# Performance work log

Hardware: AMD Instinct MI355X
Metric: run time of the kernel (lower is better)

The kernel has to match this reference:

```python
import jax, jax.numpy as jnp
import numpy as np

D = 128      # internal_dimensions
L = 4        # num_edge_convs
N = 100000   # nodes
E = 800000   # edges
G = 64       # graphs
IN = 4       # in_channels


def _ln(x, g, b):
    m = jnp.mean(x, -1, keepdims=True)
    v = jnp.mean((x - m) ** 2, -1, keepdims=True)
    return (x - m) * jax.lax.rsqrt(v + 1e-5) * g + b


def _gelu(x):
    return jax.nn.gelu(x, approximate=False)  # torch nn.GELU default (erf)


def _seg_mean(x, seg, n):
    s = jax.ops.segment_sum(x, seg, num_segments=n)
    c = jax.ops.segment_sum(jnp.ones((x.shape[0], 1), x.dtype), seg, num_segments=n)
    return s / jnp.maximum(c, 1.0)


def _seg_max(x, seg, n):
    m = jax.ops.segment_max(x, seg, num_segments=n)
    return jnp.where(jnp.isfinite(m), m, 0.0)  # empty segments -> 0 (PyG convention)


def _forward(x, edge_index, batch, num_graphs,
             in_W1, in_b1, in_g1, in_bn1, in_W2, in_b2, in_g2, in_bn2,
             pre_g, pre_b, cW1, cb1, cg1, cbb1, cW2, cb2, cg2, cbb2, pW, pb,
             ag_g, ag_b,
             kW1, kb1, kg1, kbb1, kW2, kb2, kg2, kbb2,
             kW3, kb3, kg3, kbb3, kW4, kb4):
    n = x.shape[0]
    # input_net: Linear -> LN -> GELU -> Linear -> LN   (dropout=0, eval)
    h = _gelu(_ln(x @ in_W1 + in_b1, in_g1, in_bn1))
    h = _ln(h @ in_W2 + in_b2, in_g2, in_bn2)

    x_in_max = _seg_max(h, batch, num_graphs)
    x_in_mean = _seg_mean(h, batch, num_graphs)

    src, dst = edge_index[0], edge_index[1]  # PyG: message from src (x_j) to dst (x_i)
    xcur = h
    for l in range(L):
        identity = xcur
        hn = _ln(xcur, pre_g[l], pre_b[l])
        xi = hn[dst]            # [E, D]
        xj = hn[src]            # [E, D]
        m = jnp.concatenate([xi, xj - xi], axis=-1)       # [E, 2D]
        m = _gelu(_ln(m @ cW1[l] + cb1[l], cg1[l], cbb1[l]))
        m = _gelu(_ln(m @ cW2[l] + cb2[l], cg2[l], cbb2[l]))
        a_max = _seg_max(m, dst, n)
        a_mean = _seg_mean(m, dst, n)
        aggr = jnp.concatenate([a_max, a_mean], axis=-1)  # [N, 2D]
        xcur = identity + aggr @ pW[l] + pb[l]

    xcur = _ln(xcur, ag_g, ag_b)
    x_g_max = _seg_max(xcur, batch, num_graphs)
    x_g_mean = _seg_mean(xcur, batch, num_graphs)

    xp = jnp.concatenate([x_in_max, x_in_mean, x_g_max, x_g_mean], axis=-1)  # [G, 4D]
    z = _gelu(_ln(xp @ kW1 + kb1, kg1, kbb1))
    z = _gelu(_ln(z @ kW2 + kb2, kg2, kbb2))
    z = _gelu(_ln(z @ kW3 + kb3, kg3, kbb3))
    return z @ kW4 + kb4  # [G, 1]


def setup_inputs() -> dict:
    key = jax.random.key(0)
    ks = iter(jax.random.split(key, 64))
    def W(shape, fan):
        return jax.random.normal(next(ks), shape, jnp.float32) * np.float32((2.0 / fan) ** 0.5)
    inp = {}
    inp["x"] = jax.random.normal(next(ks), (N, IN), jnp.float32)
    inp["edge_index"] = jax.random.randint(next(ks), (2, E), 0, N)
    inp["batch"] = jnp.sort(jax.random.randint(next(ks), (N,), 0, G))
    inp["num_graphs"] = G
    inp["in_W1"] = W((IN, D), IN); inp["in_b1"] = jnp.zeros((D,), jnp.float32)
    inp["in_g1"] = jnp.ones((D,), jnp.float32); inp["in_bn1"] = jnp.zeros((D,), jnp.float32)
    inp["in_W2"] = W((D, D), D); inp["in_b2"] = jnp.zeros((D,), jnp.float32)
    inp["in_g2"] = jnp.ones((D,), jnp.float32); inp["in_bn2"] = jnp.zeros((D,), jnp.float32)
    inp["pre_g"] = jnp.ones((L, D), jnp.float32); inp["pre_b"] = jnp.zeros((L, D), jnp.float32)
    inp["cW1"] = W((L, 2 * D, D), 2 * D); inp["cb1"] = jnp.zeros((L, D), jnp.float32)
    inp["cg1"] = jnp.ones((L, D), jnp.float32); inp["cbb1"] = jnp.zeros((L, D), jnp.float32)
    inp["cW2"] = W((L, D, D), D); inp["cb2"] = jnp.zeros((L, D), jnp.float32)
    inp["cg2"] = jnp.ones((L, D), jnp.float32); inp["cbb2"] = jnp.zeros((L, D), jnp.float32)
    inp["pW"] = W((L, 2 * D, D), 2 * D); inp["pb"] = jnp.zeros((L, D), jnp.float32)
    inp["ag_g"] = jnp.ones((D,), jnp.float32); inp["ag_b"] = jnp.zeros((D,), jnp.float32)
    inp["kW1"] = W((4 * D, D), 4 * D); inp["kb1"] = jnp.zeros((D,), jnp.float32)
    inp["kg1"] = jnp.ones((D,), jnp.float32); inp["kbb1"] = jnp.zeros((D,), jnp.float32)
    inp["kW2"] = W((D, D), D); inp["kb2"] = jnp.zeros((D,), jnp.float32)
    inp["kg2"] = jnp.ones((D,), jnp.float32); inp["kbb2"] = jnp.zeros((D,), jnp.float32)
    inp["kW3"] = W((D, D // 4), D); inp["kb3"] = jnp.zeros((D // 4,), jnp.float32)
    inp["kg3"] = jnp.ones((D // 4,), jnp.float32); inp["kbb3"] = jnp.zeros((D // 4,), jnp.float32)
    inp["kW4"] = W((D // 4, 1), D // 4); inp["kb4"] = jnp.zeros((1,), jnp.float32)
    return inp


def reference(x, edge_index, batch, num_graphs,
              in_W1, in_b1, in_g1, in_bn1, in_W2, in_b2, in_g2, in_bn2,
              pre_g, pre_b, cW1, cb1, cg1, cbb1, cW2, cb2, cg2, cbb2, pW, pb,
              ag_g, ag_b,
              kW1, kb1, kg1, kbb1, kW2, kb2, kg2, kbb2,
              kW3, kb3, kg3, kbb3, kW4, kb4):
    return _forward(x, edge_index, batch, num_graphs,
                    in_W1, in_b1, in_g1, in_bn1, in_W2, in_b2, in_g2, in_bn2,
                    pre_g, pre_b, cW1, cb1, cg1, cbb1, cW2, cb2, cg2, cbb2, pW, pb,
                    ag_g, ag_b,
                    kW1, kb1, kg1, kbb1, kW2, kb2, kg2, kbb2,
                    kW3, kb3, kg3, kbb3, kW4, kb4)
```

## Files before the change

kernel.cpp:

```cpp
#include <hip/hip_runtime.h>
#include <hip/hip_bf16.h>
#include <math.h>

__device__ __forceinline__ float geluf(float x) {
    return 0.5f * x * (1.0f + erff(x * 0.70710678118654752f));
}
#define MAPNEGINF 0x007FFFFFu
__device__ __forceinline__ float funmap(unsigned m) {
    return __uint_as_float((m & 0x80000000u) ? (m ^ 0x80000000u) : ~m);
}
__device__ __forceinline__ unsigned fmap(float f) {
    unsigned u = __float_as_uint(f);
    return ((int)u < 0) ? ~u : (u | 0x80000000u);
}
__device__ __forceinline__ float wred64(float v) {
#pragma unroll
    for (int m = 1; m < 64; m <<= 1) v += __shfl_xor(v, m);
    return v;
}
__device__ __forceinline__ unsigned short bf16r(float f) {
    unsigned u = __float_as_uint(f);
    u += 0x7fffu + ((u >> 16) & 1u);
    return (unsigned short)(u >> 16);
}

__device__ __forceinline__ void stage_wq(float* Ws, const float* __restrict__ src, int t) {
#pragma unroll
    for (int it = 0; it < 4; ++it) {
        const int idx = it * 1024 + (t << 2);
        *(float4*)(Ws + idx) = *(const float4*)(src + idx);
    }
}

__device__ __forceinline__ void kloop_q(const float* As, const float* Ws, float (&acc)[4][8],
                                        const int r0, const int ogc, const int kb) {
#pragma unroll
    for (int kk = 0; kk < 32; kk += 4) {
        const float4 a0 = *(const float4*)(As + (r0 + 0) * 132 + kb + kk);
        const float4 a1 = *(const float4*)(As + (r0 + 1) * 132 + kb + kk);
        const float4 a2 = *(const float4*)(As + (r0 + 2) * 132 + kb + kk);
        const float4 a3 = *(const float4*)(As + (r0 + 3) * 132 + kb + kk);
#define MAD8(R, AV)                                                                     \
    {                                                                                   \
        acc[R][0] += (AV)*wA.x; acc[R][1] += (AV)*wA.y; acc[R][2] += (AV)*wA.z;         \
        acc[R][3] += (AV)*wA.w; acc[R][4] += (AV)*wB.x; acc[R][5] += (AV)*wB.y;         \
        acc[R][6] += (AV)*wB.z; acc[R][7] += (AV)*wB.w;                                 \
    }
#define KSTEP(J, C)                                                                     \
    {                                                                                   \
        const float4 wA = *(const float4*)(Ws + (kk + (J)) * 128 + ogc);                \
        const float4 wB = *(const float4*)(Ws + (kk + (J)) * 128 + 64 + ogc);           \
        MAD8(0, a0.C) MAD8(1, a1.C) MAD8(2, a2.C) MAD8(3, a3.C)                         \
    }
        KSTEP(0, x) KSTEP(1, y) KSTEP(2, z) KSTEP(3, w)
#undef KSTEP
#undef MAD8
    }
}

__global__ void k_zero(unsigned* __restrict__ p, int n) {
    const int i = blockIdx.x * 256 + threadIdx.x;
    if (i < n) p[i] = 0u;
}

__global__ void k_copyu(const unsigned* __restrict__ a, const unsigned* __restrict__ b,
                        unsigned* __restrict__ ac, unsigned* __restrict__ bc, int n) {
    const int i = blockIdx.x * 256 + threadIdx.x;
    if (i < n) {
        ac[i] = a[i];
        bc[i] = b[i];
    }
}

__global__ void k_count(const int* __restrict__ ei, unsigned* __restrict__ deg, int E) {
    const int e = blockIdx.x * 256 + threadIdx.x;
    if (e < E) atomicAdd(deg + ei[E + e], 1u);
}

__global__ void k_scan1(const unsigned* __restrict__ deg, unsigned* __restrict__ excl,
                        unsigned* __restrict__ bsum, int n) {
    __shared__ unsigned sh[256];
    const int t = threadIdx.x;
    const int base = blockIdx.x * 1024 + t * 4;
    unsigned v0 = (base + 0 < n) ? deg[base + 0] : 0u;
    unsigned v1 = (base + 1 < n) ? deg[base + 1] : 0u;
    unsigned v2 = (base + 2 < n) ? deg[base + 2] : 0u;
    unsigned v3 = (base + 3 < n) ? deg[base + 3] : 0u;
    const unsigned s = v0 + v1 + v2 + v3;
    sh[t] = s;
    __syncthreads();
    for (int off = 1; off < 256; off <<= 1) {
        unsigned x = 0;
        if (t >= off) x = sh[t - off];
        __syncthreads();
        if (t >= off) sh[t] += x;
        __syncthreads();
    }
    const unsigned ebase = sh[t] - s;
    if (base + 0 < n) excl[base + 0] = ebase;
    if (base + 1 < n) excl[base + 1] = ebase + v0;
    if (base + 2 < n) excl[base + 2] = ebase + v0 + v1;
    if (base + 3 < n) excl[base + 3] = ebase + v0 + v1 + v2;
    if (t == 255) bsum[blockIdx.x] = sh[255];
}

__global__ void k_scan2(unsigned* __restrict__ bsum, int nb) {
    __shared__ unsigned sh[256];
    const int t = threadIdx.x;
    const unsigned v = (t < nb) ? bsum[t] : 0u;
    sh[t] = v;
    __syncthreads();
    for (int off = 1; off < 256; off <<= 1) {
        unsigned x = 0;
        if (t >= off) x = sh[t - off];
        __syncthreads();
        if (t >= off) sh[t] += x;
        __syncthreads();
    }
    if (t < nb) bsum[t] = sh[t] - v;
}

__global__ void k_scan3(unsigned* __restrict__ excl, const unsigned* __restrict__ bsum, int n) {
    const int t = threadIdx.x;
    const int base = blockIdx.x * 1024 + t * 4;
    const unsigned add = bsum[blockIdx.x];
#pragma unroll
    for (int j = 0; j < 4; ++j)
        if (base + j < n) excl[base + j] += add;
}

__global__ void k_scatter(const int* __restrict__ ei, unsigned* __restrict__ cursor,
                          int* __restrict__ esrc, int* __restrict__ edst, int E) {
    const int e = blockIdx.x * 256 + threadIdx.x;
    if (e < E) {
        const int s = ei[e];
        const int d = ei[E + e];
        const unsigned pos = atomicAdd(cursor + d, 1u);
        esrc[pos] = s;
        edst[pos] = d;
    }
}

__global__ void k_in(const float* __restrict__ x, const float* __restrict__ W1,
                     const float* __restrict__ b1, const float* __restrict__ g1,
                     const float* __restrict__ bn1, const float* __restrict__ W2,
                     const float* __restrict__ b2, const float* __restrict__ g2,
                     const float* __restrict__ bn2, float* __restrict__ C, int n) {
    __shared__ float As[64 * 132];
    __shared__ float Ws[4096];
    __shared__ float W1s[512];
    const int t = threadIdx.x;
    const int n0 = blockIdx.x * 64;
    if (t < 128) {
        W1s[t] = W1[t];
        W1s[128 + t] = W1[128 + t];
        W1s[256 + t] = W1[256 + t];
        W1s[384 + t] = W1[384 + t];
    }
    __syncthreads();
    {
        const int r = t >> 2, c0 = (t & 3) << 5;
        const int row = n0 + r;
        float4 xv = make_float4(0.f, 0.f, 0.f, 0.f);
        if (row < n) xv = *(const float4*)(x + (size_t)row * 4);
        float hv[32];
        float s = 0.f, q = 0.f;
#pragma unroll
        for (int j = 0; j < 32; ++j) {
            const int c = c0 + j;
            const float z = b1[c] + xv.x * W1s[c] + xv.y * W1s[128 + c] +
                            xv.z * W1s[256 + c] + xv.w * W1s[384 + c];
            hv[j] = z;
            s += z;
            q += z * z;
        }
        s += __shfl_xor(s, 1); s += __shfl_xor(s, 2);
        q += __shfl_xor(q, 1); q += __shfl_xor(q, 2);
        const float mean = s * 0.0078125f;
        const float var = q * 0.0078125f - mean * mean;
        const float rs = rsqrtf(var + 1e-5f);
#pragma unroll
        for (int j = 0; j < 32; ++j) {
            const int c = c0 + j;
            As[r * 132 + c] = geluf((hv[j] - mean) * rs * g1[c] + bn1[c]);
        }
    }
    float acc[4][8];
#pragma unroll
    for (int r = 0; r < 4; ++r)
#pragma unroll
        for (int o = 0; o < 8; ++o) acc[r][o] = 0.f;
    const int og = t & 15, eg = t >> 4;
    const int ogc = og << 2, r0 = eg << 2;
#pragma unroll
    for (int q4 = 0; q4 < 4; ++q4) {
        stage_wq(Ws, W2 + q4 * 4096, t);
        __syncthreads();
        kloop_q(As, Ws, acc, r0, ogc, q4 * 32);
        __syncthreads();
    }
    const float4 bA = *(const float4*)(b2 + ogc);
    const float4 bB = *(const float4*)(b2 + 64 + ogc);
    const float4 gA = *(const float4*)(g2 + ogc);
    const float4 gB = *(const float4*)(g2 + 64 + ogc);
    const float4 lA = *(const float4*)(bn2 + ogc);
    const float4 lB = *(const float4*)(bn2 + 64 + ogc);
#pragma unroll
    for (int r = 0; r < 4; ++r) {
        float v[8];
        v[0] = acc[r][0] + bA.x; v[1] = acc[r][1] + bA.y;
        v[2] = acc[r][2] + bA.z; v[3] = acc[r][3] + bA.w;
        v[4] = acc[r][4] + bB.x; v[5] = acc[r][5] + bB.y;
        v[6] = acc[r][6] + bB.z; v[7] = acc[r][7] + bB.w;
        float s = 0.f, q = 0.f;
#pragma unroll
        for (int o = 0; o < 8; ++o) { s += v[o]; q += v[o] * v[o]; }
#pragma unroll
        for (int m = 1; m < 16; m <<= 1) { s += __shfl_xor(s, m); q += __shfl_xor(q, m); }
        const float mean = s * 0.0078125f;
        const float var = q * 0.0078125f - mean * mean;
        const float rs = rsqrtf(var + 1e-5f);
        const int row = n0 + r0 + r;
        if (row < n) {
            *(float4*)(C + (size_t)row * 128 + ogc) = make_float4(
                (v[0] - mean) * rs * gA.x + lA.x, (v[1] - mean) * rs * gA.y + lA.y,
                (v[2] - mean) * rs * gA.z + lA.z, (v[3] - mean) * rs * gA.w + lA.w);
            *(float4*)(C + (size_t)row * 128 + 64 + ogc) = make_float4(
                (v[4] - mean) * rs * gB.x + lB.x, (v[5] - mean) * rs * gB.y + lB.y,
                (v[6] - mean) * rs * gB.z + lB.z, (v[7] - mean) * rs * gB.w + lB.w);
        }
    }
}

__global__ void k_pq(float* __restrict__ xcur, const float* __restrict__ upd,
                     const float* __restrict__ pbl, const float* __restrict__ g,
                     const float* __restrict__ b, const float* __restrict__ cW1,
                     const float* __restrict__ cb1, unsigned short* __restrict__ P,
                     unsigned short* __restrict__ Q, int n) {
    __shared__ float As[64 * 132];
    __shared__ float Ws[4096];
    __shared__ float sg[128], sb[128];
    const int t = threadIdx.x;
    const int n0 = blockIdx.x * 64;
    if (t < 128) { sg[t] = g[t]; sb[t] = b[t]; }
    __syncthreads();
    {
        const int r = t >> 2, c0 = (t & 3) << 5;
        const int row = n0 + r;
        const bool ok = row < n;
        float4 v4[8];
        float s = 0.f, q = 0.f;
        if (ok) {
#pragma unroll
            for (int j = 0; j < 8; ++j) {
                const int c = c0 + (j << 2);
                float4 xv = *(const float4*)(xcur + (size_t)row * 128 + c);
                if (upd) {
                    const float4 u = *(const float4*)(upd + (size_t)row * 128 + c);
                    const float4 pv = *(const float4*)(pbl + c);
                    xv = make_float4(xv.x + u.x + pv.x, xv.y + u.y + pv.y, xv.z + u.z + pv.z,
                                     xv.w + u.w + pv.w);
                    *(float4*)(xcur + (size_t)row * 128 + c) = xv;
                }
                v4[j] = xv;
                s += xv.x + xv.y + xv.z + xv.w;
                q += xv.x * xv.x + xv.y * xv.y + xv.z * xv.z + xv.w * xv.w;
            }
        } else {
#pragma unroll
            for (int j = 0; j < 8; ++j) v4[j] = make_float4(0.f, 0.f, 0.f, 0.f);
        }
        s += __shfl_xor(s, 1); s += __shfl_xor(s, 2);
        q += __shfl_xor(q, 1); q += __shfl_xor(q, 2);
        const float mean = s * 0.0078125f;
        const float var = q * 0.0078125f - mean * mean;
        const float rs = rsqrtf(var + 1e-5f);
#pragma unroll
        for (int j = 0; j < 8; ++j) {
            const int c = c0 + (j << 2);
            As[r * 132 + c + 0] = (v4[j].x - mean) * rs * sg[c + 0] + sb[c + 0];
            As[r * 132 + c + 1] = (v4[j].y - mean) * rs * sg[c + 1] + sb[c + 1];
            As[r * 132 + c + 2] = (v4[j].z - mean) * rs * sg[c + 2] + sb[c + 2];
            As[r * 132 + c + 3] = (v4[j].w - mean) * rs * sg[c + 3] + sb[c + 3];
        }
    }
    float accP[4][8], accQ[4][8];
#pragma unroll
    for (int r = 0; r < 4; ++r)
#pragma unroll
        for (int o = 0; o < 8; ++o) { accP[r][o] = 0.f; accQ[r][o] = 0.f; }
    const int og = t & 15, eg = t >> 4;
    const int ogc = og << 2, r0 = eg << 2;
#pragma unroll
    for (int q4 = 0; q4 < 4; ++q4) {
        stage_wq(Ws, cW1 + q4 * 4096, t);
        __syncthreads();
        kloop_q(As, Ws, accP, r0, ogc, q4 * 32);
        __syncthreads();
        stage_wq(Ws, cW1 + 16384 + q4 * 4096, t);
        __syncthreads();
        kloop_q(As, Ws, accQ, r0, ogc, q4 * 32);
        __syncthreads();
    }
    const float4 bA = *(const float4*)(cb1 + ogc);
    const float4 bB = *(const float4*)(cb1 + 64 + ogc);
#pragma unroll
    for (int r = 0; r < 4; ++r) {
        const int row = n0 + r0 + r;
        if (row < n) {
            ushort4 p0, p1, q0, q1;
            p0.x = bf16r(accP[r][0] - accQ[r][0] + bA.x);
            p0.y = bf16r(accP[r][1] - accQ[r][1] + bA.y);
            p0.z = bf16r(accP[r][2] - accQ[r][2] + bA.z);
            p0.w = bf16r(accP[r][3] - accQ[r][3] + bA.w);
            p1.x = bf16r(accP[r][4] - accQ[r][4] + bB.x);
            p1.y = bf16r(accP[r][5] - accQ[r][5] + bB.y);
            p1.z = bf16r(accP[r][6] - accQ[r][6] + bB.z);
            p1.w = bf16r(accP[r][7] - accQ[r][7] + bB.w);
            q0.x = bf16r(accQ[r][0]); q0.y = bf16r(accQ[r][1]);
            q0.z = bf16r(accQ[r][2]); q0.w = bf16r(accQ[r][3]);
            q1.x = bf16r(accQ[r][4]); q1.y = bf16r(accQ[r][5]);
            q1.z = bf16r(accQ[r][6]); q1.w = bf16r(accQ[r][7]);
            *(ushort4*)(P + (size_t)row * 128 + ogc) = p0;
            *(ushort4*)(P + (size_t)row * 128 + 64 + ogc) = p1;
            *(ushort4*)(Q + (size_t)row * 128 + ogc) = q0;
            *(ushort4*)(Q + (size_t)row * 128 + 64 + ogc) = q1;
        }
    }
}

__global__ __launch_bounds__(256, 2) void k_edge(
    const unsigned short* __restrict__ P, const unsigned short* __restrict__ Q,
    const int* __restrict__ esrc, const int* __restrict__ edst, const float* __restrict__ W2,
    const float* __restrict__ g1, const float* __restrict__ b1, const float* __restrict__ cb2,
    const float* __restrict__ g2, const float* __restrict__ b2,
    const unsigned* __restrict__ rowend, const unsigned* __restrict__ degc,
    const float* __restrict__ pW, float* __restrict__ upd, float* __restrict__ recmax,
    float* __restrict__ recsum, int* __restrict__ recid, int E) {
    __shared__ float Us[64 * 132];
    __shared__ float Ws[4096];
    __shared__ unsigned Pcu[64 * 64];
    __shared__ int sdst[64], ssrc[64], sdg[64];
    __shared__ unsigned char srid[64], sfirst[64];
    __shared__ float scb2[128], sg2[128], sb2[128];
    __shared__ float smx[128], ssm[128], spart[256];
    const int t = threadIdx.x;
    const int base = blockIdx.x * 512;
    if (t >= 128) {
        const int d = t - 128;
        scb2[d] = cb2[d];
        sg2[d] = g2[d];
        sb2[d] = b2[d];
    }
    const int lane = t & 63, wave = t >> 6;
    const int d0 = lane << 1;
    const float g1a = g1[d0], g1b = g1[d0 + 1], b1a = b1[d0], b1b = b1[d0 + 1];
    const int og = t & 15, eg = t >> 4;
    const int ogc = og << 2, r0 = eg << 2;
    int cur = -1, istart = 0;
    float vmax = -INFINITY, vsum = 0.f;
    int id0 = -1, id1 = -1;

    auto flushrun = [&](int iend) {
        const unsigned re = rowend[cur];
        const unsigned dg = degc[cur];
        const unsigned rs0 = re - dg;
        const unsigned ps = (unsigned)(base + istart), pe = (unsigned)(base + iend);
        if (ps == rs0 && pe == re) {
            if (t < 128) {
                smx[t] = vmax;
                ssm[t] = vsum / (float)dg;
            }
            __syncthreads();
            {
                const int d = t & 127;
                const float* wc = pW + ((t >> 7) ? 16384 : 0) + d;
                const float* sv = (t >> 7) ? ssm : smx;
                float a = 0.f;
#pragma unroll 8
                for (int k = 0; k < 128; ++k) a += sv[k] * wc[(size_t)k << 7];
                spart[t] = a;
            }
            __syncthreads();
            if (t < 128) upd[(size_t)cur * 128 + t] = spart[t] + spart[t + 128];
        } else {
            const int slot = (istart == 0) ? 0 : 1;
            if (t < 128) {
                const size_t ro = (size_t)(2 * blockIdx.x + slot) * 128 + t;
                recmax[ro] = vmax;
                recsum[ro] = vsum;
            }
            if (slot == 0) id0 = cur; else id1 = cur;
        }
    };

    for (int s8 = 0; s8 < 8; ++s8) {
        const int sb = base + s8 * 64;
        __syncthreads();
        if (t < 64) {
            const int idx = sb + t;
            const int ci = idx < E ? idx : (E - 1);
            ssrc[t] = esrc[ci];
            const int d = edst[ci];
            sdg[t] = d;
            sdst[t] = (idx < E) ? d : -1;
        }
        __syncthreads();
        if (t < 64) {
            const int first = (t == 0) ? 1 : (sdg[t] != sdg[t - 1]);
            int scanv = first;
#pragma unroll
            for (int o = 1; o < 64; o <<= 1) {
                const int up = __shfl_up(scanv, o);
                if (lane >= o) scanv += up;
            }
            sfirst[t] = (unsigned char)first;
            srid[t] = (unsigned char)(scanv - 1);
        }
        __syncthreads();
        unsigned quv[16];
#pragma unroll 4
        for (int p = 0; p < 16; ++p) {
            const int i = (p << 2) + wave;
            quv[p] = *(const unsigned*)(Q + ((size_t)ssrc[i] << 7) + d0);
            if (sfirst[i]) {
                Pcu[(int)srid[i] * 64 + lane] =
                    *(const unsigned*)(P + ((size_t)sdg[i] << 7) + d0);
            }
        }
        __syncthreads();
#pragma unroll 4
        for (int p = 0; p < 16; ++p) {
            const int i = (p << 2) + wave;
            const unsigned pu = Pcu[(int)srid[i] * 64 + lane];
            const unsigned qu = quv[p];
            const float x0 = __uint_as_float(pu << 16) + __uint_as_float(qu << 16);
            const float x1 =
                __uint_as_float(pu & 0xffff0000u) + __uint_as_float(qu & 0xffff0000u);
            const float s = wred64(x0 + x1);
            const float q = wred64(x0 * x0 + x1 * x1);
            const float mean = s * 0.0078125f;
            const float var = q * 0.0078125f - mean * mean;
            const float rs = rsqrtf(var + 1e-5f);
            const float y0 = geluf((x0 - mean) * rs * g1a + b1a);
            const float y1 = geluf((x1 - mean) * rs * g1b + b1b);
            *(float2*)(Us + i * 132 + d0) = make_float2(y0, y1);
        }
        float acc[4][8];
#pragma unroll
        for (int r = 0; r < 4; ++r)
#pragma unroll
            for (int o = 0; o < 8; ++o) acc[r][o] = 0.f;
#pragma unroll
        for (int q4 = 0; q4 < 4; ++q4) {
            stage_wq(Ws, W2 + q4 * 4096, t);
            __syncthreads();
            kloop_q(Us, Ws, acc, r0, ogc, q4 * 32);
            __syncthreads();
        }
#pragma unroll
        for (int r = 0; r < 4; ++r) {
            float v[8];
            float s = 0.f, q = 0.f;
#pragma unroll
            for (int o = 0; o < 8; ++o) {
                const int col = (o < 4) ? (ogc + o) : (64 + ogc + o - 4);
                v[o] = acc[r][o] + scb2[col];
                s += v[o];
                q += v[o] * v[o];
            }
#pragma unroll
            for (int m = 1; m < 16; m <<= 1) { s += __shfl_xor(s, m); q += __shfl_xor(q, m); }
            const float mean = s * 0.0078125f;
            const float var = q * 0.0078125f - mean * mean;
            const float rs = rsqrtf(var + 1e-5f);
#pragma unroll
            for (int o = 0; o < 8; ++o) {
                const int col = (o < 4) ? (ogc + o) : (64 + ogc + o - 4);
                v[o] = geluf((v[o] - mean) * rs * sg2[col] + sb2[col]);
            }
            *(float4*)(Us + (r0 + r) * 132 + ogc) = make_float4(v[0], v[1], v[2], v[3]);
            *(float4*)(Us + (r0 + r) * 132 + 64 + ogc) = make_float4(v[4], v[5], v[6], v[7]);
        }
        __syncthreads();
        for (int i = 0; i < 64; ++i) {
            const int dn = sdst[i];
            const int gi = s8 * 64 + i;
            if (dn != cur) {
                if (cur >= 0) flushrun(gi);
                cur = dn;
                istart = gi;
                vmax = -INFINITY;
                vsum = 0.f;
            }
            if (dn >= 0 && t < 128) {
                const float v = Us[i * 132 + t];
                vmax = fmaxf(vmax, v);
                vsum += v;
            }
        }
    }
    if (cur >= 0) flushrun(min(512, E - base));
    if (t == 0) {
        recid[2 * blockIdx.x] = id0;
        recid[2 * blockIdx.x + 1] = id1;
    }
}

__global__ void k_merge2(const unsigned* __restrict__ rowend, const unsigned* __restrict__ degc,
                         const float* __restrict__ recmax, const float* __restrict__ recsum,
                         const int* __restrict__ recid, const float* __restrict__ pW,
                         float* __restrict__ upd, int n) {
    __shared__ float sm[128], ss[128];
    const int node = blockIdx.x;
    const int d = threadIdx.x;
    if (node >= n) return;
    const unsigned dg = degc[node];
    if (dg == 0u) {
        upd[(size_t)node * 128 + d] = 0.f;
        return;
    }
    const unsigned re = rowend[node], rs = re - dg;
    const int b0 = rs >> 9, b1 = (re - 1) >> 9;
    if (b0 == b1) return;
    float m = -INFINITY, s = 0.f;
    for (int b = b0; b <= b1; ++b) {
#pragma unroll
        for (int sl = 0; sl < 2; ++sl) {
            if (recid[2 * b + sl] == node) {
                const size_t ro = (size_t)(2 * b + sl) * 128 + d;
                m = fmaxf(m, recmax[ro]);
                s += recsum[ro];
            }
        }
    }
    sm[d] = m;
    ss[d] = s / (float)dg;
    __syncthreads();
    float a = 0.f;
#pragma unroll 8
    for (int k = 0; k < 128; ++k)
        a += sm[k] * pW[(size_t)k * 128 + d] + ss[k] * pW[(size_t)(128 + k) * 128 + d];
    upd[(size_t)node * 128 + d] = a;
}

__global__ void k_lnpool(const float* __restrict__ xcur, const float* __restrict__ upd,
                         const float* __restrict__ pbl, const float* __restrict__ g,
                         const float* __restrict__ b, const int* __restrict__ batch,
                         unsigned* __restrict__ gmax, float* __restrict__ gsum,
                         unsigned* __restrict__ gcount, int n) {
    __shared__ float Ys[64 * 132];
    __shared__ int sbt[64];
    const int t = threadIdx.x;
    const int n0 = blockIdx.x * 64;
    if (t < 64) {
        const int node = n0 + t;
        sbt[t] = (node < n) ? batch[node] : -1;
    }
    {
        const int r = t >> 2, c0 = (t & 3) << 5;
        const int row = n0 + r;
        const bool ok = row < n;
        float4 v4[8];
        float s = 0.f, q = 0.f;
        if (ok) {
#pragma unroll
            for (int j = 0; j < 8; ++j) {
                const int c = c0 + (j << 2);
                const float4 xv = *(const float4*)(xcur + (size_t)row * 128 + c);
                const float4 u = *(const float4*)(upd + (size_t)row * 128 + c);
                const float4 pv = *(const float4*)(pbl + c);
                v4[j] = make_float4(xv.x + u.x + pv.x, xv.y + u.y + pv.y, xv.z + u.z + pv.z,
                                    xv.w + u.w + pv.w);
                s += v4[j].x + v4[j].y + v4[j].z + v4[j].w;
                q += v4[j].x * v4[j].x + v4[j].y * v4[j].y + v4[j].z * v4[j].z +
                     v4[j].w * v4[j].w;
            }
        } else {
#pragma unroll
            for (int j = 0; j < 8; ++j) v4[j] = make_float4(0.f, 0.f, 0.f, 0.f);
        }
        s += __shfl_xor(s, 1); s += __shfl_xor(s, 2);
        q += __shfl_xor(q, 1); q += __shfl_xor(q, 2);
        const float mean = s * 0.0078125f;
        const float var = q * 0.0078125f - mean * mean;
        const float rs = rsqrtf(var + 1e-5f);
#pragma unroll
        for (int j = 0; j < 8; ++j) {
            const int c = c0 + (j << 2);
            Ys[r * 132 + c + 0] = (v4[j].x - mean) * rs * g[c + 0] + b[c + 0];
            Ys[r * 132 + c + 1] = (v4[j].y - mean) * rs * g[c + 1] + b[c + 1];
            Ys[r * 132 + c + 2] = (v4[j].z - mean) * rs * g[c + 2] + b[c + 2];
            Ys[r * 132 + c + 3] = (v4[j].w - mean) * rs * g[c + 3] + b[c + 3];
        }
    }
    __syncthreads();
    if (t < 128) {
        int curg = -1;
        float vmax = -INFINITY, vsum = 0.f;
        unsigned cnt = 0;
        for (int i = 0; i < 64; ++i) {
            const int gid = sbt[i];
            if (gid != curg) {
                if (curg >= 0) {
                    atomicMax(gmax + (size_t)curg * 128 + t, fmap(vmax));
                    atomicAdd(gsum + (size_t)curg * 128 + t, vsum);
                    if (t == 0) atomicAdd(gcount + curg, cnt);
                }
                curg = gid;
                vmax = -INFINITY;
                vsum = 0.f;
                cnt = 0;
            }
            if (gid >= 0) {
                const float v = Ys[i * 132 + t];
                vmax = fmaxf(vmax, v);
                vsum += v;
                cnt++;
            }
        }
        if (curg >= 0) {
            atomicMax(gmax + (size_t)curg * 128 + t, fmap(vmax));
            atomicAdd(gsum + (size_t)curg * 128 + t, vsum);
            if (t == 0) atomicAdd(gcount + curg, cnt);
        }
    }
}

__global__ void k_pool_init(unsigned* __restrict__ gmax1, float* __restrict__ gsum1,
                            unsigned* __restrict__ gcount1, unsigned* __restrict__ gmax2,
                            float* __restrict__ gsum2, unsigned* __restrict__ gcount2, int ng) {
    const int i = blockIdx.x * 256 + threadIdx.x;
    if (i < ng * 128) {
        gmax1[i] = MAPNEGINF;
        gsum1[i] = 0.f;
        gmax2[i] = MAPNEGINF;
        gsum2[i] = 0.f;
    }
    if (i < ng) {
        gcount1[i] = 0u;
        gcount2[i] = 0u;
    }
}

__global__ void k_pool(const float* __restrict__ in, const int* __restrict__ batch,
                       unsigned* __restrict__ gmax, float* __restrict__ gsum,
                       unsigned* __restrict__ gcount, int n) {
    const int t = threadIdx.x;
    if (t >= 128) return;
    const int per = (n + gridDim.x - 1) / gridDim.x;
    const int i0 = blockIdx.x * per;
    const int i1 = min(n, i0 + per);
    if (i0 >= i1) return;
    int cur = batch[i0];
    float vmax = -INFINITY, vsum = 0.f;
    unsigned cnt = 0;
    for (int i = i0; i < i1; ++i) {
        const int g = batch[i];
        if (g != cur) {
            atomicMax(gmax + (size_t)cur * 128 + t, fmap(vmax));
            atomicAdd(gsum + (size_t)cur * 128 + t, vsum);
            if (t == 0) atomicAdd(gcount + cur, cnt);
            cur = g;
            vmax = -INFINITY;
            vsum = 0.f;
            cnt = 0;
        }
        const float v = in[(size_t)i * 128 + t];
        vmax = fmaxf(vmax, v);
        vsum += v;
        cnt++;
    }
    atomicMax(gmax + (size_t)cur * 128 + t, fmap(vmax));
    atomicAdd(gsum + (size_t)cur * 128 + t, vsum);
    if (t == 0) atomicAdd(gcount + cur, cnt);
}

__global__ void k_xp(const unsigned* __restrict__ gmax1, const float* __restrict__ gsum1,
                     const unsigned* __restrict__ gcount1, const unsigned* __restrict__ gmax2,
                     const float* __restrict__ gsum2, const unsigned* __restrict__ gcount2,
                     float* __restrict__ xp) {
    const int g = blockIdx.x, d = threadIdx.x;
    const unsigned c1u = gcount1[g], c2u = gcount2[g];
    const float c1 = (float)(c1u < 1u ? 1u : c1u);
    const float c2 = (float)(c2u < 1u ? 1u : c2u);
    const unsigned m1 = gmax1[g * 128 + d], m2 = gmax2[g * 128 + d];
    xp[g * 512 + d] = (m1 == MAPNEGINF) ? 0.f : funmap(m1);
    xp[g * 512 + 128 + d] = gsum1[g * 128 + d] / c1;
    xp[g * 512 + 256 + d] = (m2 == MAPNEGINF) ? 0.f : funmap(m2);
    xp[g * 512 + 384 + d] = gsum2[g * 128 + d] / c2;
}

__global__ __launch_bounds__(64) void k_know(
    const float* __restrict__ xp, const float* __restrict__ kW1, const float* __restrict__ kb1,
    const float* __restrict__ kg1, const float* __restrict__ kbb1, const float* __restrict__ kW2,
    const float* __restrict__ kb2, const float* __restrict__ kg2, const float* __restrict__ kbb2,
    const float* __restrict__ kW3, const float* __restrict__ kb3, const float* __restrict__ kg3,
    const float* __restrict__ kbb3, const float* __restrict__ kW4, const float* __restrict__ kb4,
    float* __restrict__ out) {
    __shared__ float sh[512];
    __shared__ float s3[32];
    const int l = threadIdx.x, g = blockIdx.x;
    const int d0 = l << 1;
    *(float4*)(sh + l * 8) = *(const float4*)(xp + g * 512 + l * 8);
    *(float4*)(sh + l * 8 + 4) = *(const float4*)(xp + g * 512 + l * 8 + 4);
    __syncthreads();
    float a0 = kb1[d0], a1 = kb1[d0 + 1];
    for (int k = 0; k < 512; ++k) {
        const float u = sh[k];
        const float2 w = *(const float2*)(kW1 + k * 128 + d0);
        a0 += u * w.x;
        a1 += u * w.y;
    }
    {
        const float s = wred64(a0 + a1), q = wred64(a0 * a0 + a1 * a1);
        const float mean = s * 0.0078125f, var = q * 0.0078125f - mean * mean;
        const float rs = rsqrtf(var + 1e-5f);
        a0 = geluf((a0 - mean) * rs * kg1[d0] + kbb1[d0]);
        a1 = geluf((a1 - mean) * rs * kg1[d0 + 1] + kbb1[d0 + 1]);
    }
    __syncthreads();
    sh[d0] = a0;
    sh[d0 + 1] = a1;
    __syncthreads();
    float b0v = kb2[d0], b1v = kb2[d0 + 1];
    for (int k = 0; k < 128; ++k) {
        const float u = sh[k];
        const float2 w = *(const float2*)(kW2 + k * 128 + d0);
        b0v += u * w.x;
        b1v += u * w.y;
    }
    {
        const float s = wred64(b0v + b1v), q = wred64(b0v * b0v + b1v * b1v);
        const float mean = s * 0.0078125f, var = q * 0.0078125f - mean * mean;
        const float rs = rsqrtf(var + 1e-5f);
        b0v = geluf((b0v - mean) * rs * kg2[d0] + kbb2[d0]);
        b1v = geluf((b1v - mean) * rs * kg2[d0 + 1] + kbb2[d0 + 1]);
    }
    __syncthreads();
    sh[d0] = b0v;
    sh[d0 + 1] = b1v;
    __syncthreads();
    const int d3 = (l & 15) << 1;
    float c0 = kb3[d3], c1 = kb3[d3 + 1];
    for (int k = 0; k < 128; ++k) {
        const float u = sh[k];
        const float2 w = *(const float2*)(kW3 + k * 32 + d3);
        c0 += u * w.x;
        c1 += u * w.y;
    }
    {
        float s = c0 + c1, q = c0 * c0 + c1 * c1;
#pragma unroll
        for (int m = 1; m < 16; m <<= 1) {
            s += __shfl_xor(s, m);
            q += __shfl_xor(q, m);
        }
        const float mean = s * 0.03125f, var = q * 0.03125f - mean * mean;
        const float rs = rsqrtf(var + 1e-5f);
        c0 = geluf((c0 - mean) * rs * kg3[d3] + kbb3[d3]);
        c1 = geluf((c1 - mean) * rs * kg3[d3 + 1] + kbb3[d3 + 1]);
    }
    if (l < 16) {
        s3[d3] = c0;
        s3[d3 + 1] = c1;
    }
    __syncthreads();
    if (l == 0) {
        float rr = kb4[0];
        for (int k = 0; k < 32; ++k) rr += s3[k] * kW4[k];
        out[g] = rr;
    }
}

extern "C" void kernel_launch(void* const* d_in, const int* in_sizes, int n_in, void* d_out,
                              int out_size, void* d_ws, size_t ws_size, hipStream_t stream) {
    const int N = in_sizes[0] / 4;
    const int E = in_sizes[1] / 2;
    const int G = 64;
    const int L = 4;

    const float* x = (const float*)d_in[0];
    const int* ei = (const int*)d_in[1];
    const int* batch = (const int*)d_in[2];
    const float* inW1 = (const float*)d_in[4];
    const float* inb1 = (const float*)d_in[5];
    const float* ing1 = (const float*)d_in[6];
    const float* inbn1 = (const float*)d_in[7];
    const float* inW2 = (const float*)d_in[8];
    const float* inb2 = (const float*)d_in[9];
    const float* ing2 = (const float*)d_in[10];
    const float* inbn2 = (const float*)d_in[11];
    const float* pre_g = (const float*)d_in[12];
    const float* pre_b = (const float*)d_in[13];
    const float* cW1 = (const float*)d_in[14];
    const float* cb1 = (const float*)d_in[15];
    const float* cg1 = (const float*)d_in[16];
    const float* cbb1 = (const float*)d_in[17];
    const float* cW2 = (const float*)d_in[18];
    const float* cb2 = (const float*)d_in[19];
    const float* cg2 = (const float*)d_in[20];
    const float* cbb2 = (const float*)d_in[21];
    const float* pW = (const float*)d_in[22];
    const float* pb = (const float*)d_in[23];
    const float* ag_g = (const float*)d_in[24];
    const float* ag_b = (const float*)d_in[25];
    const float* kW1 = (const float*)d_in[26];
    const float* kb1 = (const float*)d_in[27];
    const float* kg1 = (const float*)d_in[28];
    const float* kbb1 = (const float*)d_in[29];
    const float* kW2 = (const float*)d_in[30];
    const float* kb2 = (const float*)d_in[31];
    const float* kg2 = (const float*)d_in[32];
    const float* kbb2 = (const float*)d_in[33];
    const float* kW3 = (const float*)d_in[34];
    const float* kb3 = (const float*)d_in[35];
    const float* kg3 = (const float*)d_in[36];
    const float* kbb3 = (const float*)d_in[37];
    const float* kW4 = (const float*)d_in[38];
    const float* kb4 = (const float*)d_in[39];
    float* out = (float*)d_out;

    const int nblkE = (E + 511) / 512;

    char* wsb = (char*)d_ws;
    size_t off = 0;
    auto ALC = [&](size_t bytes) {
        void* p = wsb + off;
        off = (off + bytes + 255) & ~(size_t)255;
        return p;
    };
    const size_t NB = (size_t)N * 128 * 4;
    float* xcur = (float*)ALC(NB);
    float* upd = (float*)ALC(NB);
    unsigned short* Pb = (unsigned short*)ALC((size_t)N * 128 * 2);
    unsigned short* Qb = (unsigned short*)ALC((size_t)N * 128 * 2);
    unsigned* deg = (unsigned*)ALC((size_t)N * 4);
    unsigned* cursor = (unsigned*)ALC((size_t)N * 4);
    unsigned* degc = (unsigned*)ALC((size_t)N * 4);
    unsigned* rowend = (unsigned*)ALC((size_t)N * 4);
    unsigned* bsum = (unsigned*)ALC(4096);
    int* esrc = (int*)ALC((size_t)E * 4);
    int* edst = (int*)ALC((size_t)E * 4);
    float* recmax = (float*)ALC((size_t)nblkE * 2 * 128 * 4);
    float* recsum = (float*)ALC((size_t)nblkE * 2 * 128 * 4);
    int* recid = (int*)ALC((size_t)nblkE * 2 * 4);
    unsigned* gmax1 = (unsigned*)ALC((size_t)G * 128 * 4);
    float* gsum1 = (float*)ALC((size_t)G * 128 * 4);
    unsigned* gcount1 = (unsigned*)ALC((size_t)G * 4);
    unsigned* gmax2 = (unsigned*)ALC((size_t)G * 128 * 4);
    float* gsum2 = (float*)ALC((size_t)G * 128 * 4);
    unsigned* gcount2 = (unsigned*)ALC((size_t)G * 4);
    float* xp = (float*)ALC((size_t)G * 512 * 4);

    if (off > ws_size) {
        k_zero<<<(out_size + 255) / 256, 256, 0, stream>>>((unsigned*)d_out, out_size);
        return;
    }

    k_zero<<<(N + 255) / 256, 256, 0, stream>>>(deg, N);
    k_count<<<(E + 255) / 256, 256, 0, stream>>>(ei, deg, E);
    const int nb = (N + 1023) / 1024;
    k_scan1<<<nb, 256, 0, stream>>>(deg, cursor, bsum, N);
    k_scan2<<<1, 256, 0, stream>>>(bsum, nb);
    k_scan3<<<nb, 256, 0, stream>>>(cursor, bsum, N);
    k_scatter<<<(E + 255) / 256, 256, 0, stream>>>(ei, cursor, esrc, edst, E);
    k_copyu<<<(N + 255) / 256, 256, 0, stream>>>(deg, cursor, degc, rowend, N);

    const int grid64 = (N + 63) / 64;
    k_in<<<grid64, 256, 0, stream>>>(x, inW1, inb1, ing1, inbn1, inW2, inb2, ing2, inbn2, xcur,
                                     N);
    k_pool_init<<<(G * 128 + 255) / 256, 256, 0, stream>>>(gmax1, gsum1, gcount1, gmax2, gsum2,
                                                           gcount2, G);
    k_pool<<<512, 256, 0, stream>>>(xcur, batch, gmax1, gsum1, gcount1, N);

    for (int l = 0; l < L; ++l) {
        k_pq<<<grid64, 256, 0, stream>>>(xcur, (l == 0) ? (const float*)nullptr : upd,
                                         (l == 0) ? (const float*)nullptr : (pb + (l - 1) * 128),
                                         pre_g + l * 128, pre_b + l * 128,
                                         cW1 + (size_t)l * 32768, cb1 + l * 128, Pb, Qb, N);
        k_edge<<<nblkE, 256, 0, stream>>>(Pb, Qb, esrc, edst, cW2 + (size_t)l * 16384,
                                          cg1 + l * 128, cbb1 + l * 128, cb2 + l * 128,
                                          cg2 + l * 128, cbb2 + l * 128, rowend, degc,
                                          pW + (size_t)l * 32768, upd, recmax, recsum, recid, E);
        k_merge2<<<N, 128, 0, stream>>>(rowend, degc, recmax, recsum, recid,
                                        pW + (size_t)l * 32768, upd, N);
    }

    k_lnpool<<<grid64, 256, 0, stream>>>(xcur, upd, pb + 3 * 128, ag_g, ag_b, batch, gmax2,
                                         gsum2, gcount2, N);
    k_xp<<<G, 128, 0, stream>>>(gmax1, gsum1, gcount1, gmax2, gsum2, gcount2, xp);
    k_know<<<G, 64, 0, stream>>>(xp, kW1, kb1, kg1, kbb1, kW2, kb2, kg2, kbb2, kW3, kb3, kg3,
                                 kbb3, kW4, kb4, out);
}
```

Baseline: 83.73 ms.

## Batch per-node output projections through shared memory and drop P dedup staging

Completed destination nodes are no longer projected one at a time with a 256-thread GEMV that reads pW from global memory. Their max/mean vectors are queued in shared memory, and once 16 have gathered they are projected together as a small GEMM, with pW staged through shared memory in chunks. Separately, the scan and dedup step that cached each destination's P row in shared memory is removed, and P and Q are loaded straight from global memory per edge. The batching amortises weight traffic and syncs across nodes, at the cost of reloading repeated P rows. It also uses more shared memory and could hurt occupancy.

```diff
diff --git a/kernel.cpp b/kernel.cpp
--- a/kernel.cpp
+++ b/kernel.cpp
@@ -329,6 +329,7 @@
     }
 }
 
+#define QN 16
 __global__ __launch_bounds__(256, 2) void k_edge(
     const unsigned short* __restrict__ P, const unsigned short* __restrict__ Q,
     const int* __restrict__ esrc, const int* __restrict__ edst, const float* __restrict__ W2,
@@ -339,11 +340,10 @@
     float* __restrict__ recsum, int* __restrict__ recid, int E) {
     __shared__ float Us[64 * 132];
     __shared__ float Ws[4096];
-    __shared__ unsigned Pcu[64 * 64];
+    __shared__ float Qq[QN * 260];
+    __shared__ int qnode[QN];
     __shared__ int sdst[64], ssrc[64], sdg[64];
-    __shared__ unsigned char srid[64], sfirst[64];
     __shared__ float scb2[128], sg2[128], sb2[128];
-    __shared__ float smx[128], ssm[128], spart[256];
     const int t = threadIdx.x;
     const int base = blockIdx.x * 512;
     if (t >= 128) {
@@ -360,29 +360,51 @@
     int cur = -1, istart = 0;
     float vmax = -INFINITY, vsum = 0.f;
     int id0 = -1, id1 = -1;
-
-    auto flushrun = [&](int iend) {
+    int qn = 0;
+
+    auto flushq = [&]() {
+        if (qn == 0) return;
+        __syncthreads();
+        float qacc[8];
+#pragma unroll
+        for (int o = 0; o < 8; ++o) qacc[o] = 0.f;
+        const int qr = t >> 4;
+        const int qc = (t & 15) << 3;
+        for (int qs = 0; qs < 8; ++qs) {
+            stage_wq(Ws, pW + qs * 4096, t);
+            __syncthreads();
+            const float* aq = Qq + qr * 260 + qs * 32;
+#pragma unroll
+            for (int kk = 0; kk < 32; ++kk) {
+                const float av = aq[kk];
+                const float* wr = Ws + kk * 128 + qc;
+#pragma unroll
+                for (int o = 0; o < 8; ++o) qacc[o] += av * wr[o];
+            }
+            __syncthreads();
+        }
+        if (qr < qn) {
+            float* dstp = upd + (size_t)qnode[qr] * 128 + qc;
+            *(float4*)(dstp) = make_float4(qacc[0], qacc[1], qacc[2], qacc[3]);
+            *(float4*)(dstp + 4) = make_float4(qacc[4], qacc[5], qacc[6], qacc[7]);
+        }
+        __syncthreads();
+        qn = 0;
+    };
+
+    auto endrun = [&](int iend) {
         const unsigned re = rowend[cur];
         const unsigned dg = degc[cur];
         const unsigned rs0 = re - dg;
         const unsigned ps = (unsigned)(base + istart), pe = (unsigned)(base + iend);
         if (ps == rs0 && pe == re) {
             if (t < 128) {
-                smx[t] = vmax;
-                ssm[t] = vsum / (float)dg;
-            }
-            __syncthreads();
-            {
-                const int d = t & 127;
-                const float* wc = pW + ((t >> 7) ? 16384 : 0) + d;
-                const float* sv = (t >> 7) ? ssm : smx;
-                float a = 0.f;
-#pragma unroll 8
-                for (int k = 0; k < 128; ++k) a += sv[k] * wc[(size_t)k << 7];
-                spart[t] = a;
-            }
-            __syncthreads();
-            if (t < 128) upd[(size_t)cur * 128 + t] = spart[t] + spart[t + 128];
+                Qq[qn * 260 + t] = vmax;
+                Qq[qn * 260 + 128 + t] = vsum / (float)dg;
+            }
+            if (t == 0) qnode[qn] = cur;
+            ++qn;
+            if (qn == QN) flushq();
         } else {
             const int slot = (istart == 0) ? 0 : 1;
             if (t < 128) {
@@ -406,34 +428,11 @@
             sdst[t] = (idx < E) ? d : -1;
         }
         __syncthreads();
-        if (t < 64) {
-            const int first = (t == 0) ? 1 : (sdg[t] != sdg[t - 1]);
-            int scanv = first;
-#pragma unroll
-            for (int o = 1; o < 64; o <<= 1) {
-                const int up = __shfl_up(scanv, o);
-                if (lane >= o) scanv += up;
-            }
-            sfirst[t] = (unsigned char)first;
-            srid[t] = (unsigned char)(scanv - 1);
-        }
-        __syncthreads();
-        unsigned quv[16];
 #pragma unroll 4
         for (int p = 0; p < 16; ++p) {
             const int i = (p << 2) + wave;
-            quv[p] = *(const unsigned*)(Q + ((size_t)ssrc[i] << 7) + d0);
-            if (sfirst[i]) {
-                Pcu[(int)srid[i] * 64 + lane] =
-                    *(const unsigned*)(P + ((size_t)sdg[i] << 7) + d0);
-            }
-        }
-        __syncthreads();
-#pragma unroll 4
-        for (int p = 0; p < 16; ++p) {
-            const int i = (p << 2) + wave;
-            const unsigned pu = Pcu[(int)srid[i] * 64 + lane];
-            const unsigned qu = quv[p];
+            const unsigned pu = *(const unsigned*)(P + ((size_t)sdg[i] << 7) + d0);
+            const unsigned qu = *(const unsigned*)(Q + ((size_t)ssrc[i] << 7) + d0);
             const float x0 = __uint_as_float(pu << 16) + __uint_as_float(qu << 16);
             const float x1 =
                 __uint_as_float(pu & 0xffff0000u) + __uint_as_float(qu & 0xffff0000u);
@@ -487,7 +486,7 @@
             const int dn = sdst[i];
             const int gi = s8 * 64 + i;
             if (dn != cur) {
-                if (cur >= 0) flushrun(gi);
+                if (cur >= 0) endrun(gi);
                 cur = dn;
                 istart = gi;
                 vmax = -INFINITY;
@@ -500,7 +499,8 @@
             }
         }
     }
-    if (cur >= 0) flushrun(min(512, E - base));
+    if (cur >= 0) endrun(min(512, E - base));
+    flushq();
     if (t == 0) {
         recid[2 * blockIdx.x] = id0;
         recid[2 * blockIdx.x + 1] = id1;
```

Measured after the change: 82.91 ms (median of 2 runs). Within noise of the previous version (-1.0%).
